# Kernel tuning notes

Hardware: AMD Instinct MI355X
Metric: run time of the kernel (lower is better)

## Reference

```python
import jax, jax.numpy as jnp
import numpy as np

B, H, W, N, DX, DZ = 4, 64, 64, 4096, 2, 128
INIT_LS = 0.1


def setup_inputs() -> dict:
    key = jax.random.key(0)
    k1, k2, k3, k4 = jax.random.split(key, 4)
    xc_off_grid = jax.random.uniform(k1, (B, N, DX), dtype=jnp.float32)
    # regular grid coordinates in [0, 1]^2, broadcast over batch
    gy, gx = jnp.meshgrid(jnp.linspace(0.0, 1.0, H), jnp.linspace(0.0, 1.0, W), indexing="ij")
    xc_on_grid = jnp.broadcast_to(jnp.stack([gy, gx], axis=-1)[None], (B, H, W, DX)).astype(jnp.float32)
    zc_off_grid = jax.random.normal(k2, (B, N, DZ), dtype=jnp.float32)
    zc_on_grid = jax.random.normal(k3, (B, H, W, DZ), dtype=jnp.float32)
    # lengthscale_param = log(exp(init_lengthscale) - 1)  (inverse softplus)
    lengthscale_param = jnp.log(jnp.expm1(jnp.full((DX,), INIT_LS, dtype=jnp.float32)))
    return {
        "xc_off_grid": xc_off_grid,
        "xc_on_grid": xc_on_grid,
        "zc_off_grid": zc_off_grid,
        "zc_on_grid": zc_on_grid,
        "lengthscale_param": lengthscale_param,
        "ignore_on_grid": 0,
    }


def reference(xc_off_grid, xc_on_grid, zc_off_grid, zc_on_grid, lengthscale_param, ignore_on_grid):
    b = xc_on_grid.shape[0]
    grid_shape = xc_on_grid.shape[1:-1]
    dz = zc_off_grid.shape[-1]
    xg = xc_on_grid.reshape(b, -1, xc_on_grid.shape[-1])  # [b, m, dx]
    lengthscale = 1e-05 + jax.nn.softplus(lengthscale_param)  # [dx]
    # squared scaled distances: [b, m, n]
    diff = (xg[:, :, None, :] - xc_off_grid[:, None, :, :]) / lengthscale
    weights = jnp.exp(-0.5 * jnp.sum(diff * diff, axis=-1))  # [b, m, n]
    zc = jnp.einsum("bmn,bnd->bmd", weights, zc_off_grid)  # [b, m, dz]
    if not ignore_on_grid:
        zc = zc + zc_on_grid.reshape(b, -1, dz)
    return zc.reshape((b,) + grid_shape + (dz,))
```

## Files before the change

kernel.cpp:

```cpp
#include <hip/hip_runtime.h>

#define HH 64
#define WW 64
#define NN 4096
#define DZc 128
#define KS 8
#define KRANGE (NN / KS)
#define NSTEP (KRANGE / 16)
#define CELLS 2097152
#define WS_NEED (8ull * CELLS * 2ull)

typedef __fp16 v2fp16 __attribute__((ext_vector_type(2)));
typedef _Float16 v4h __attribute__((ext_vector_type(4)));
typedef _Float16 v8h __attribute__((ext_vector_type(8)));
typedef float v16f __attribute__((ext_vector_type(16)));

__device__ __forceinline__ unsigned pk16(float lo, float hi){
  union { v2fp16 h; unsigned u; } c;
  c.h = __builtin_amdgcn_cvt_pkrtz(lo, hi);
  return c.u;
}
__device__ __forceinline__ float fexp2(float x){ return __builtin_amdgcn_exp2f(x); }

__global__ void init_out_kernel(const float4* __restrict__ zc_on,
                                const int* __restrict__ ignore,
                                float4* __restrict__ out){
  int i = blockIdx.x * blockDim.x + threadIdx.x;
  float4 v = zc_on[i];
  if (ignore[0]) { v.x = 0.f; v.y = 0.f; v.z = 0.f; v.w = 0.f; }
  out[i] = v;
}

__global__ void reduce_kernel(const v4h* __restrict__ part,
                              const float4* __restrict__ zc_on,
                              const int* __restrict__ ignore,
                              float4* __restrict__ out){
  int i = blockIdx.x * blockDim.x + threadIdx.x;
  float4 s = zc_on[i];
  if (ignore[0]) { s.x = 0.f; s.y = 0.f; s.z = 0.f; s.w = 0.f; }
  #pragma unroll
  for (int ks = 0; ks < KS; ++ks){
    v4h p = part[(size_t)ks * (CELLS / 4) + i];
    s.x += (float)p[0]; s.y += (float)p[1]; s.z += (float)p[2]; s.w += (float)p[3];
  }
  out[i] = s;
}

__global__ __launch_bounds__(256, 4)
void setconv_gemm_kernel(const float* __restrict__ xc_off,
                         const float* __restrict__ xc_on,
                         const float* __restrict__ zc_off,
                         const float* __restrict__ lsp,
                         _Float16* __restrict__ part,
                         float* __restrict__ out)
{
  __shared__ unsigned short gt[24 * 520];

  const int tid = threadIdx.x;
  const int bid = blockIdx.x;
  const int ks  = bid >> 7;
  const int rem = bid & 127;
  const int b   = rem >> 5;
  const int mt  = rem & 31;
  const int iy0 = (mt >> 3) * 16;
  const int ix0 = (mt & 7) * 8;
  const int nbase = ks * KRANGE;

  const float lsy = 1e-5f + log1pf(expf(lsp[0]));
  const float lsx = 1e-5f + log1pf(expf(lsp[1]));
  const float LOG2E = 1.44269504088896340736f;
  const float ay = -0.5f * LOG2E / (lsy * lsy);
  const float ax = -0.5f * LOG2E / (lsx * lsx);

  const float* xb = xc_off + (size_t)b * NN * 2;
  const float* zb = zc_off + (size_t)b * NN * DZc;

  {
    const int g  = tid >> 5;
    const int p8 = tid & 31;
    float cc[3], aa[3];
    #pragma unroll
    for (int rr = 0; rr < 3; ++rr){
      int r = 3 * g + rr;
      if (r < 16){ cc[rr] = xc_on[((b * HH + iy0 + r) * WW) * 2];          aa[rr] = ay; }
      else       { cc[rr] = xc_on[(b * HH * WW + ix0 + (r - 16)) * 2 + 1]; aa[rr] = ax; }
    }
    unsigned* gtw = (unsigned*)gt;
    #pragma unroll
    for (int j = 0; j < 8; ++j){
      const int p = p8 + 32 * j;
      float4 xq = *(const float4*)&xb[(size_t)(nbase + 2 * p) * 2];
      #pragma unroll
      for (int rr = 0; rr < 3; ++rr){
        int r = 3 * g + rr;
        float s0 = (r < 16) ? xq.x : xq.y;
        float s1 = (r < 16) ? xq.z : xq.w;
        float d0 = cc[rr] - s0, d1 = cc[rr] - s1;
        gtw[r * 260 + p] = pk16(fexp2(aa[rr] * d0 * d0), fexp2(aa[rr] * d1 * d1));
      }
    }
  }
  __syncthreads();

  const int lane = tid & 63;
  const int wv  = tid >> 6;
  const int wm  = wv >> 1;
  const int wdh = wv & 1;
  const int l31 = lane & 31;
  const int lh  = lane >> 5;
  const int gxr  = 16 + (l31 & 7);
  const int gyr0 = wm * 8 + (l31 >> 3);

  v16f acc[2][2];
  #pragma unroll
  for (int m = 0; m < 2; ++m)
    #pragma unroll
    for (int d = 0; d < 2; ++d)
      #pragma unroll
      for (int r = 0; r < 16; ++r)
        acc[m][d][r] = 0.f;

  const float* zp0 = zb + (size_t)(nbase + lh * 8) * DZc + wdh * 64 + l31;

  float pend[16];
  #pragma unroll
  for (int dtl = 0; dtl < 2; ++dtl)
    #pragma unroll
    for (int j = 0; j < 8; ++j)
      pend[dtl * 8 + j] = zp0[j * DZc + dtl * 32];

  #pragma unroll 1
  for (int s = 0; s < NSTEP; ++s){
    const int k0 = s * 16 + lh * 8;

    v8h bfr[2];
    #pragma unroll
    for (int dtl = 0; dtl < 2; ++dtl){
      union { unsigned u[4]; v8h v; } u;
      #pragma unroll
      for (int jj = 0; jj < 4; ++jj)
        u.u[jj] = pk16(pend[dtl * 8 + 2 * jj], pend[dtl * 8 + 2 * jj + 1]);
      bfr[dtl] = u.v;
    }

    if (s + 1 < NSTEP){
      const float* zp = zp0 + (size_t)(s + 1) * 16 * DZc;
      #pragma unroll
      for (int dtl = 0; dtl < 2; ++dtl)
        #pragma unroll
        for (int j = 0; j < 8; ++j)
          pend[dtl * 8 + j] = zp[j * DZc + dtl * 32];
    }

    const v8h gx = *(const v8h*)&gt[gxr * 520 + k0];
    #pragma unroll
    for (int mtl = 0; mtl < 2; ++mtl){
      const v8h gy = *(const v8h*)&gt[(gyr0 + mtl * 4) * 520 + k0];
      v8h av = gy * gx;
      #pragma unroll
      for (int dtl = 0; dtl < 2; ++dtl)
        acc[mtl][dtl] = __builtin_amdgcn_mfma_f32_32x32x16_f16(av, bfr[dtl], acc[mtl][dtl], 0, 0, 0);
    }
  }

  if (part){
    _Float16* pw = part + (size_t)ks * CELLS;
    #pragma unroll
    for (int mtl = 0; mtl < 2; ++mtl)
      #pragma unroll
      for (int dtl = 0; dtl < 2; ++dtl){
        const int d = wdh * 64 + dtl * 32 + l31;
        #pragma unroll
        for (int reg = 0; reg < 16; ++reg){
          const int row = (reg & 3) + 8 * (reg >> 2) + 4 * lh;
          const int m = wm * 64 + mtl * 32 + row;
          const int iy = iy0 + (m >> 3);
          const int ix = ix0 + (m & 7);
          pw[((b * HH + iy) * WW + ix) * DZc + d] = (_Float16)acc[mtl][dtl][reg];
        }
      }
  } else {
    #pragma unroll
    for (int mtl = 0; mtl < 2; ++mtl)
      #pragma unroll
      for (int dtl = 0; dtl < 2; ++dtl){
        const int d = wdh * 64 + dtl * 32 + l31;
        #pragma unroll
        for (int reg = 0; reg < 16; ++reg){
          const int row = (reg & 3) + 8 * (reg >> 2) + 4 * lh;
          const int m = wm * 64 + mtl * 32 + row;
          const int iy = iy0 + (m >> 3);
          const int ix = ix0 + (m & 7);
          unsafeAtomicAdd(&out[((b * HH + iy) * WW + ix) * DZc + d], acc[mtl][dtl][reg]);
        }
      }
  }
}

extern "C" void kernel_launch(void* const* d_in, const int* in_sizes, int n_in,
                              void* d_out, int out_size, void* d_ws, size_t ws_size,
                              hipStream_t stream){
  const float* xc_off = (const float*)d_in[0];
  const float* xc_on  = (const float*)d_in[1];
  const float* zc_off = (const float*)d_in[2];
  const float* zc_on  = (const float*)d_in[3];
  const float* lsp    = (const float*)d_in[4];
  const int*   ign    = (const int*)d_in[5];
  float* out = (float*)d_out;

  if (ws_size >= WS_NEED){
    _Float16* part = (_Float16*)d_ws;
    setconv_gemm_kernel<<<KS * 128, 256, 0, stream>>>(xc_off, xc_on, zc_off, lsp, part, out);
    reduce_kernel<<<CELLS / 4 / 256, 256, 0, stream>>>((const v4h*)part, (const float4*)zc_on, ign, (float4*)out);
  } else {
    init_out_kernel<<<out_size / 1024, 256, 0, stream>>>((const float4*)zc_on, ign, (float4*)out);
    setconv_gemm_kernel<<<KS * 128, 256, 0, stream>>>(xc_off, xc_on, zc_off, lsp, nullptr, out);
  }
}
```

Before: 116.8 us.

## Cache zc operand in registers and loop over four m-tiles per block

```diff
diff --git a/kernel.cpp b/kernel.cpp
--- a/kernel.cpp
+++ b/kernel.cpp
@@ -4,11 +4,11 @@
 #define WW 64
 #define NN 4096
 #define DZc 128
-#define KS 8
+#define KS 16
 #define KRANGE (NN / KS)
 #define NSTEP (KRANGE / 16)
 #define CELLS 2097152
-#define WS_NEED (8ull * CELLS * 2ull)
+#define WS_NEED ((unsigned long long)KS * CELLS * 2ull)
 
 typedef __fp16 v2fp16 __attribute__((ext_vector_type(2)));
 typedef _Float16 v4h __attribute__((ext_vector_type(4)));
@@ -46,7 +46,7 @@
   out[i] = s;
 }
 
-__global__ __launch_bounds__(256, 4)
+__global__ __launch_bounds__(256, 2)
 void setconv_gemm_kernel(const float* __restrict__ xc_off,
                          const float* __restrict__ xc_on,
                          const float* __restrict__ zc_off,
@@ -54,16 +54,14 @@
                          _Float16* __restrict__ part,
                          float* __restrict__ out)
 {
-  __shared__ unsigned short gt[24 * 520];
+  __shared__ unsigned short gt[24 * 264];
 
   const int tid = threadIdx.x;
   const int bid = blockIdx.x;
-  const int ks  = bid >> 7;
-  const int rem = bid & 127;
-  const int b   = rem >> 5;
-  const int mt  = rem & 31;
-  const int iy0 = (mt >> 3) * 16;
-  const int ix0 = (mt & 7) * 8;
+  const int ks  = bid >> 5;
+  const int rem = bid & 31;
+  const int b   = rem >> 3;
+  const int mg  = rem & 7;
   const int nbase = ks * KRANGE;
 
   const float lsy = 1e-5f + log1pf(expf(lsp[0]));
@@ -74,33 +72,6 @@
 
   const float* xb = xc_off + (size_t)b * NN * 2;
   const float* zb = zc_off + (size_t)b * NN * DZc;
-
-  {
-    const int g  = tid >> 5;
-    const int p8 = tid & 31;
-    float cc[3], aa[3];
-    #pragma unroll
-    for (int rr = 0; rr < 3; ++rr){
-      int r = 3 * g + rr;
-      if (r < 16){ cc[rr] = xc_on[((b * HH + iy0 + r) * WW) * 2];          aa[rr] = ay; }
-      else       { cc[rr] = xc_on[(b * HH * WW + ix0 + (r - 16)) * 2 + 1]; aa[rr] = ax; }
-    }
-    unsigned* gtw = (unsigned*)gt;
-    #pragma unroll
-    for (int j = 0; j < 8; ++j){
-      const int p = p8 + 32 * j;
-      float4 xq = *(const float4*)&xb[(size_t)(nbase + 2 * p) * 2];
-      #pragma unroll
-      for (int rr = 0; rr < 3; ++rr){
-        int r = 3 * g + rr;
-        float s0 = (r < 16) ? xq.x : xq.y;
-        float s1 = (r < 16) ? xq.z : xq.w;
-        float d0 = cc[rr] - s0, d1 = cc[rr] - s1;
-        gtw[r * 260 + p] = pk16(fexp2(aa[rr] * d0 * d0), fexp2(aa[rr] * d1 * d1));
-      }
-    }
-  }
-  __syncthreads();
 
   const int lane = tid & 63;
   const int wv  = tid >> 6;
@@ -111,89 +82,146 @@
   const int gxr  = 16 + (l31 & 7);
   const int gyr0 = wm * 8 + (l31 >> 3);
 
-  v16f acc[2][2];
+  const float* zp0 = zb + (size_t)(nbase + lh * 8) * DZc + wdh * 64 + l31;
+  v8h breg[32];
+  float pa[16], pb[16];
+  {
+    #pragma unroll
+    for (int dtl = 0; dtl < 2; ++dtl)
+      #pragma unroll
+      for (int j = 0; j < 8; ++j)
+        pa[dtl * 8 + j] = zp0[j * DZc + dtl * 32];
+  }
   #pragma unroll
-  for (int m = 0; m < 2; ++m)
+  for (int sp = 0; sp < 8; ++sp){
+    {
+      const float* zp = zp0 + (size_t)(2 * sp + 1) * 16 * DZc;
+      #pragma unroll
+      for (int dtl = 0; dtl < 2; ++dtl)
+        #pragma unroll
+        for (int j = 0; j < 8; ++j)
+          pb[dtl * 8 + j] = zp[j * DZc + dtl * 32];
+    }
+    {
+      #pragma unroll
+      for (int dtl = 0; dtl < 2; ++dtl){
+        union { unsigned u[4]; v8h v; } w;
+        #pragma unroll
+        for (int jj = 0; jj < 4; ++jj)
+          w.u[jj] = pk16(pa[dtl * 8 + 2 * jj], pa[dtl * 8 + 2 * jj + 1]);
+        breg[dtl * 16 + 2 * sp] = w.v;
+      }
+    }
+    if (sp < 7){
+      const float* zp = zp0 + (size_t)(2 * sp + 2) * 16 * DZc;
+      #pragma unroll
+      for (int dtl = 0; dtl < 2; ++dtl)
+        #pragma unroll
+        for (int j = 0; j < 8; ++j)
+          pa[dtl * 8 + j] = zp[j * DZc + dtl * 32];
+    }
+    {
+      #pragma unroll
+      for (int dtl = 0; dtl < 2; ++dtl){
+        union { unsigned u[4]; v8h v; } w;
+        #pragma unroll
+        for (int jj = 0; jj < 4; ++jj)
+          w.u[jj] = pk16(pb[dtl * 8 + 2 * jj], pb[dtl * 8 + 2 * jj + 1]);
+        breg[dtl * 16 + 2 * sp + 1] = w.v;
+      }
+    }
+  }
+
+  #pragma unroll 1
+  for (int it = 0; it < 4; ++it){
+    const int mt  = mg * 4 + it;
+    const int iy0 = (mt >> 3) * 16;
+    const int ix0 = (mt & 7) * 8;
+
+    __syncthreads();
+
+    {
+      const int g  = tid >> 5;
+      const int p8 = tid & 31;
+      float cc[3], aa[3];
+      #pragma unroll
+      for (int rr = 0; rr < 3; ++rr){
+        int r = 3 * g + rr;
+        if (r < 16){ cc[rr] = xc_on[((b * HH + iy0 + r) * WW) * 2];          aa[rr] = ay; }
+        else       { cc[rr] = xc_on[(b * HH * WW + ix0 + (r - 16)) * 2 + 1]; aa[rr] = ax; }
+      }
+      unsigned* gtw = (unsigned*)gt;
+      #pragma unroll
+      for (int j = 0; j < 4; ++j){
+        const int p = p8 + 32 * j;
+        float4 xq = *(const float4*)&xb[(size_t)(nbase + 2 * p) * 2];
+        #pragma unroll
+        for (int rr = 0; rr < 3; ++rr){
+          int r = 3 * g + rr;
+          float s0 = (r < 16) ? xq.x : xq.y;
+          float s1 = (r < 16) ? xq.z : xq.w;
+          float d0 = cc[rr] - s0, d1 = cc[rr] - s1;
+          gtw[r * 132 + p] = pk16(fexp2(aa[rr] * d0 * d0), fexp2(aa[rr] * d1 * d1));
+        }
+      }
+    }
+    __syncthreads();
+
+    v16f acc[2][2];
     #pragma unroll
-    for (int d = 0; d < 2; ++d)
-      #pragma unroll
-      for (int r = 0; r < 16; ++r)
-        acc[m][d][r] = 0.f;
-
-  const float* zp0 = zb + (size_t)(nbase + lh * 8) * DZc + wdh * 64 + l31;
-
-  float pend[16];
-  #pragma unroll
-  for (int dtl = 0; dtl < 2; ++dtl)
+    for (int m = 0; m < 2; ++m)
+      #pragma unroll
+      for (int d = 0; d < 2; ++d)
+        #pragma unroll
+        for (int r = 0; r < 16; ++r)
+          acc[m][d][r] = 0.f;
+
     #pragma unroll
-    for (int j = 0; j < 8; ++j)
-      pend[dtl * 8 + j] = zp0[j * DZc + dtl * 32];
-
-  #pragma unroll 1
-  for (int s = 0; s < NSTEP; ++s){
-    const int k0 = s * 16 + lh * 8;
-
-    v8h bfr[2];
-    #pragma unroll
-    for (int dtl = 0; dtl < 2; ++dtl){
-      union { unsigned u[4]; v8h v; } u;
-      #pragma unroll
-      for (int jj = 0; jj < 4; ++jj)
-        u.u[jj] = pk16(pend[dtl * 8 + 2 * jj], pend[dtl * 8 + 2 * jj + 1]);
-      bfr[dtl] = u.v;
-    }
-
-    if (s + 1 < NSTEP){
-      const float* zp = zp0 + (size_t)(s + 1) * 16 * DZc;
-      #pragma unroll
-      for (int dtl = 0; dtl < 2; ++dtl)
-        #pragma unroll
-        for (int j = 0; j < 8; ++j)
-          pend[dtl * 8 + j] = zp[j * DZc + dtl * 32];
-    }
-
-    const v8h gx = *(const v8h*)&gt[gxr * 520 + k0];
-    #pragma unroll
-    for (int mtl = 0; mtl < 2; ++mtl){
-      const v8h gy = *(const v8h*)&gt[(gyr0 + mtl * 4) * 520 + k0];
-      v8h av = gy * gx;
-      #pragma unroll
-      for (int dtl = 0; dtl < 2; ++dtl)
-        acc[mtl][dtl] = __builtin_amdgcn_mfma_f32_32x32x16_f16(av, bfr[dtl], acc[mtl][dtl], 0, 0, 0);
-    }
-  }
-
-  if (part){
-    _Float16* pw = part + (size_t)ks * CELLS;
-    #pragma unroll
-    for (int mtl = 0; mtl < 2; ++mtl)
-      #pragma unroll
-      for (int dtl = 0; dtl < 2; ++dtl){
-        const int d = wdh * 64 + dtl * 32 + l31;
-        #pragma unroll
-        for (int reg = 0; reg < 16; ++reg){
-          const int row = (reg & 3) + 8 * (reg >> 2) + 4 * lh;
-          const int m = wm * 64 + mtl * 32 + row;
-          const int iy = iy0 + (m >> 3);
-          const int ix = ix0 + (m & 7);
-          pw[((b * HH + iy) * WW + ix) * DZc + d] = (_Float16)acc[mtl][dtl][reg];
+    for (int s = 0; s < NSTEP; ++s){
+      const int k0 = s * 16 + lh * 8;
+      const v8h gx = *(const v8h*)&gt[gxr * 264 + k0];
+      #pragma unroll
+      for (int mtl = 0; mtl < 2; ++mtl){
+        const v8h gy = *(const v8h*)&gt[(gyr0 + mtl * 4) * 264 + k0];
+        v8h av = gy * gx;
+        #pragma unroll
+        for (int dtl = 0; dtl < 2; ++dtl)
+          acc[mtl][dtl] = __builtin_amdgcn_mfma_f32_32x32x16_f16(av, breg[dtl * 16 + s], acc[mtl][dtl], 0, 0, 0);
+      }
+    }
+
+    if (part){
+      _Float16* pw = part + (size_t)ks * CELLS;
+      #pragma unroll
+      for (int mtl = 0; mtl < 2; ++mtl)
+        #pragma unroll
+        for (int dtl = 0; dtl < 2; ++dtl){
+          const int d = wdh * 64 + dtl * 32 + l31;
+          #pragma unroll
+          for (int reg = 0; reg < 16; ++reg){
+            const int row = (reg & 3) + 8 * (reg >> 2) + 4 * lh;
+            const int m = wm * 64 + mtl * 32 + row;
+            const int iy = iy0 + (m >> 3);
+            const int ix = ix0 + (m & 7);
+            pw[((b * HH + iy) * WW + ix) * DZc + d] = (_Float16)acc[mtl][dtl][reg];
+          }
         }
-      }
-  } else {
-    #pragma unroll
-    for (int mtl = 0; mtl < 2; ++mtl)
-      #pragma unroll
-      for (int dtl = 0; dtl < 2; ++dtl){
-        const int d = wdh * 64 + dtl * 32 + l31;
-        #pragma unroll
-        for (int reg = 0; reg < 16; ++reg){
-          const int row = (reg & 3) + 8 * (reg >> 2) + 4 * lh;
-          const int m = wm * 64 + mtl * 32 + row;
-          const int iy = iy0 + (m >> 3);
-          const int ix = ix0 + (m & 7);
-          unsafeAtomicAdd(&out[((b * HH + iy) * WW + ix) * DZc + d], acc[mtl][dtl][reg]);
+    } else {
+      #pragma unroll
+      for (int mtl = 0; mtl < 2; ++mtl)
+        #pragma unroll
+        for (int dtl = 0; dtl < 2; ++dtl){
+          const int d = wdh * 64 + dtl * 32 + l31;
+          #pragma unroll
+          for (int reg = 0; reg < 16; ++reg){
+            const int row = (reg & 3) + 8 * (reg >> 2) + 4 * lh;
+            const int m = wm * 64 + mtl * 32 + row;
+            const int iy = iy0 + (m >> 3);
+            const int ix = ix0 + (m & 7);
+            unsafeAtomicAdd(&out[((b * HH + iy) * WW + ix) * DZc + d], acc[mtl][dtl][reg]);
+          }
         }
-      }
+    }
   }
 }
 
@@ -210,10 +238,10 @@
 
   if (ws_size >= WS_NEED){
     _Float16* part = (_Float16*)d_ws;
-    setconv_gemm_kernel<<<KS * 128, 256, 0, stream>>>(xc_off, xc_on, zc_off, lsp, part, out);
+    setconv_gemm_kernel<<<KS * 32, 256, 0, stream>>>(xc_off, xc_on, zc_off, lsp, part, out);
     reduce_kernel<<<CELLS / 4 / 256, 256, 0, stream>>>((const v4h*)part, (const float4*)zc_on, ign, (float4*)out);
   } else {
     init_out_kernel<<<out_size / 1024, 256, 0, stream>>>((const float4*)zc_on, ign, (float4*)out);
-    setconv_gemm_kernel<<<KS * 128, 256, 0, stream>>>(xc_off, xc_on, zc_off, lsp, nullptr, out);
-  }
-}
+    setconv_gemm_kernel<<<KS * 32, 256, 0, stream>>>(xc_off, xc_on, zc_off, lsp, nullptr, out);
+  }
+}
```

New measurement: 167.8 us. +43.7%, slower.
